# Optimization experiments

Measured on AMD Instinct MI355X. Metric: run time of the kernel, lower is better.

## Reference

```python
import math
import jax, jax.numpy as jnp
import numpy as np

D_MODEL = 1024
NUM_HEADS = 16
HEAD_DIM = D_MODEL // NUM_HEADS
MAX_REL = 128


def setup_inputs() -> dict:
    key = jax.random.key(0)
    ks = jax.random.split(key, 7)
    B, S = 2, 2048
    s = 1.0 / math.sqrt(D_MODEL)
    return {
        "x": jax.random.normal(ks[0], (B, S, D_MODEL), dtype=jnp.float32),
        "mask": jnp.ones((B, S, S), dtype=jnp.int32),
        "w_q": jax.random.normal(ks[1], (D_MODEL, D_MODEL), dtype=jnp.float32) * s,
        "w_k": jax.random.normal(ks[2], (D_MODEL, D_MODEL), dtype=jnp.float32) * s,
        "w_v": jax.random.normal(ks[3], (D_MODEL, D_MODEL), dtype=jnp.float32) * s,
        "w_o_w": jax.random.normal(ks[4], (D_MODEL, D_MODEL), dtype=jnp.float32) * s,
        "w_o_b": jnp.zeros((D_MODEL,), dtype=jnp.float32),
        "rel_emb": jax.random.normal(ks[5], (2 * MAX_REL + 1, HEAD_DIM), dtype=jnp.float32),
    }


def reference(x, mask, w_q, w_k, w_v, w_o_w, w_o_b, rel_emb):
    B, S, D = x.shape
    H, hd = NUM_HEADS, HEAD_DIM
    scale = math.sqrt(hd)

    def proj(w):  # torch Linear: x @ w.T  -> [B,H,S,hd]
        return (x @ w.T).reshape(B, S, H, hd).transpose(0, 2, 1, 3)

    Q, K, V = proj(w_q), proj(w_k), proj(w_v)

    # content scores (scaled)
    scores = jnp.einsum("bhqd,bhkd->bhqk", Q, K) / scale

    # T5-style relative position bias (NOT scaled, matching source)
    pos = jnp.arange(S)
    dist = jnp.clip(pos[None, :] - pos[:, None], -MAX_REL, MAX_REL) + MAX_REL  # [S,S]
    rel = rel_emb[dist]  # [S,S,hd]
    scores = scores + jnp.einsum("bhqd,qkd->bhqk", Q, rel)

    scores = jnp.where(mask[:, None, :, :] == 0, -1e9, scores)
    attn = jax.nn.softmax(scores, axis=-1)  # [B,H,S,S]

    ctx = jnp.einsum("bhqk,bhkd->bhqd", attn, V)
    ctx = ctx.transpose(0, 2, 1, 3).reshape(B, S, D)
    out = ctx @ w_o_w.T + w_o_b
    return out, attn
```

## Files before the change

kernel.cpp:

```cpp
#include <hip/hip_runtime.h>
#include <hip/hip_bf16.h>

#define B_ 2
#define S_ 2048
#define H_ 16
#define HD_ 64
#define D_ 1024
#define NJ_ 257
#define RSTRIDE_ 264

typedef __bf16 v8bf __attribute__((ext_vector_type(8)));
typedef __bf16 v4bf __attribute__((ext_vector_type(4)));
typedef float  v4f  __attribute__((ext_vector_type(4)));

static __device__ __forceinline__ v4f mfma16(v8bf a, v8bf b, v4f c) {
    return __builtin_amdgcn_mfma_f32_16x16x32_bf16(a, b, c, 0, 0, 0);
}

__global__ void k_split2(const float* __restrict__ src, __bf16* __restrict__ h,
                         __bf16* __restrict__ l, int n4) {
    int i = blockIdx.x * blockDim.x + threadIdx.x;
    int stride = gridDim.x * blockDim.x;
    for (; i < n4; i += stride) {
        const float4 v = ((const float4*)src)[i];
        float vv[4] = {v.x, v.y, v.z, v.w};
        v4bf hv, lv;
#pragma unroll
        for (int j = 0; j < 4; j++) {
            __bf16 hb = (__bf16)vv[j];
            hv[j] = hb;
            lv[j] = (__bf16)(vv[j] - (float)hb);
        }
        *(v4bf*)(h + 4 * (size_t)i) = hv;
        *(v4bf*)(l + 4 * (size_t)i) = lv;
    }
}

__global__ void k_cast4(const float* __restrict__ w0, const float* __restrict__ w1,
                        const float* __restrict__ w2, const float* __restrict__ w3,
                        __bf16* __restrict__ o0, __bf16* __restrict__ o1,
                        __bf16* __restrict__ o2, __bf16* __restrict__ o3) {
    const int n4each = (D_ * D_) / 4;
    int i = blockIdx.x * blockDim.x + threadIdx.x;
    int stride = gridDim.x * blockDim.x;
    for (; i < 4 * n4each; i += stride) {
        const int region = i >> 18, j = i & (n4each - 1);
        const float* src = region == 0 ? w0 : region == 1 ? w1 : region == 2 ? w2 : w3;
        __bf16* dst = region == 0 ? o0 : region == 1 ? o1 : region == 2 ? o2 : o3;
        const float4 v = ((const float4*)src)[j];
        v4bf o = {(__bf16)v.x, (__bf16)v.y, (__bf16)v.z, (__bf16)v.w};
        *(v4bf*)(dst + 4 * (size_t)j) = o;
    }
}

__global__ void k_rowflag(const int* __restrict__ mask, unsigned char* __restrict__ flags) {
    const int row = blockIdx.x;
    const int4* mp = (const int4*)(mask + (size_t)row * S_);
    int ok = 1;
    for (int i = threadIdx.x; i < S_ / 4; i += blockDim.x) {
        int4 m = mp[i];
        ok &= (m.x != 0) & (m.y != 0) & (m.z != 0) & (m.w != 0);
    }
    int all = __syncthreads_and(ok);
    if (threadIdx.x == 0) flags[row] = (unsigned char)(all != 0);
}

__global__ __launch_bounds__(256) void k_projQKV(const __bf16* __restrict__ xh,
                                                 const __bf16* __restrict__ xl,
                                                 const __bf16* __restrict__ wqh,
                                                 const __bf16* __restrict__ wkh,
                                                 const __bf16* __restrict__ wvh,
                                                 __bf16* __restrict__ Qh,
                                                 __bf16* __restrict__ Ql,
                                                 __bf16* __restrict__ Kh,
                                                 __bf16* __restrict__ Vb) {
    __shared__ __bf16 sXh[64][72], sXl[64][72], sW[64][72];
    const int seg = blockIdx.x >> 4;
    const int n0 = (blockIdx.x & 15) * 64;
    const int m0 = blockIdx.y * 64;
    const __bf16* W = seg == 0 ? wqh : (seg == 1 ? wkh : wvh);
    const int tid = threadIdx.x, lane = tid & 63, wid = tid >> 6;
    const int fr = lane & 15, fo = (lane >> 4) * 8;
    const int srow = tid >> 2, scol = (tid & 3) * 16;
    v4f acc[4] = {};
    for (int k0 = 0; k0 < D_; k0 += 64) {
        const size_t ga = (size_t)(m0 + srow) * D_ + k0 + scol;
        const size_t gb = (size_t)(n0 + srow) * D_ + k0 + scol;
        *(v8bf*)&sXh[srow][scol]     = *(const v8bf*)(xh + ga);
        *(v8bf*)&sXh[srow][scol + 8] = *(const v8bf*)(xh + ga + 8);
        if (seg < 2) {
            *(v8bf*)&sXl[srow][scol]     = *(const v8bf*)(xl + ga);
            *(v8bf*)&sXl[srow][scol + 8] = *(const v8bf*)(xl + ga + 8);
        }
        *(v8bf*)&sW[srow][scol]     = *(const v8bf*)(W + gb);
        *(v8bf*)&sW[srow][scol + 8] = *(const v8bf*)(W + gb + 8);
        __syncthreads();
#pragma unroll
        for (int ks = 0; ks < 2; ks++) {
            v8bf ah = *(const v8bf*)&sXh[wid * 16 + fr][ks * 32 + fo];
            v8bf al;
            if (seg < 2) al = *(const v8bf*)&sXl[wid * 16 + fr][ks * 32 + fo];
#pragma unroll
            for (int nt = 0; nt < 4; nt++) {
                v8bf bb = *(const v8bf*)&sW[nt * 16 + fr][ks * 32 + fo];
                acc[nt] = mfma16(ah, bb, acc[nt]);
                if (seg < 2) acc[nt] = mfma16(al, bb, acc[nt]);
            }
        }
        __syncthreads();
    }
#pragma unroll
    for (int nt = 0; nt < 4; nt++) {
#pragma unroll
        for (int r = 0; r < 4; r++) {
            const int row = m0 + wid * 16 + (lane >> 4) * 4 + r;
            const int col = n0 + nt * 16 + fr;
            const size_t idx = (size_t)row * D_ + col;
            const float f = acc[nt][r];
            if (seg == 0) {
                __bf16 hb = (__bf16)f;
                Qh[idx] = hb;
                Ql[idx] = (__bf16)(f - (float)hb);
            } else if (seg == 1) {
                Kh[idx] = (__bf16)f;
            } else {
                Vb[idx] = (__bf16)f;
            }
        }
    }
}

__global__ __launch_bounds__(256) void k_vtrans(const __bf16* __restrict__ Vb,
                                                __bf16* __restrict__ Vt) {
    __shared__ __bf16 t[64][72];
    const int s0 = blockIdx.x * 64, n0 = blockIdx.y * 64, b = blockIdx.z;
    const int tid = threadIdx.x;
    const int r = tid >> 2, c = (tid & 3) * 16;
    const size_t gin = ((size_t)(b * S_ + s0 + r)) * D_ + n0 + c;
    *(v8bf*)&t[r][c]     = *(const v8bf*)(Vb + gin);
    *(v8bf*)&t[r][c + 8] = *(const v8bf*)(Vb + gin + 8);
    __syncthreads();
    v8bf o0, o1;
#pragma unroll
    for (int j = 0; j < 8; j++) { o0[j] = t[c + j][r]; o1[j] = t[c + 8 + j][r]; }
    const size_t gout = ((size_t)(b * D_ + n0 + r)) * S_ + s0 + c;
    *(v8bf*)(Vt + gout)     = o0;
    *(v8bf*)(Vt + gout + 8) = o1;
}

__global__ __launch_bounds__(256) void k_relgemm(const __bf16* __restrict__ Qh,
                                                 const __bf16* __restrict__ Ql,
                                                 const __bf16* __restrict__ relh,
                                                 const __bf16* __restrict__ rell,
                                                 float* __restrict__ Rg,
                                                 float* __restrict__ qnorm,
                                                 float* __restrict__ Rmax) {
    const int q0 = blockIdx.x * 64;
    const int bh = blockIdx.y;
    const int b = bh >> 4, h = bh & 15;
    const int tid = threadIdx.x, lane = tid & 63, wid = tid >> 6;
    const int fr = lane & 15, fo = (lane >> 4) * 8;
    const size_t qbase = (size_t)(b * S_ + q0 + wid * 16 + fr) * D_ + h * HD_;
    v8bf qa_h[2], qa_l[2];
#pragma unroll
    for (int ks = 0; ks < 2; ks++) {
        qa_h[ks] = *(const v8bf*)(Qh + qbase + ks * 32 + fo);
        qa_l[ks] = *(const v8bf*)(Ql + qbase + ks * 32 + fo);
    }

    float qs = 0.0f;
#pragma unroll
    for (int ks = 0; ks < 2; ks++)
#pragma unroll
        for (int j = 0; j < 8; j++) {
            const float v = (float)qa_h[ks][j] + (float)qa_l[ks][j];
            qs += v * v;
        }
    qs += __shfl_xor(qs, 16);
    qs += __shfl_xor(qs, 32);
    if ((lane >> 4) == 0) qnorm[(size_t)bh * S_ + q0 + wid * 16 + fr] = sqrtf(qs);

    v4f acc[17] = {};
#pragma unroll
    for (int jt = 0; jt < 17; jt++) {
        int j = jt * 16 + fr;
        if (j > 256) j = 256;
        const size_t rb = (size_t)j * HD_;
#pragma unroll
        for (int ks = 0; ks < 2; ks++) {
            v8bf bh_ = *(const v8bf*)(relh + rb + ks * 32 + fo);
            v8bf bl_ = *(const v8bf*)(rell + rb + ks * 32 + fo);
            acc[jt] = mfma16(qa_h[ks], bh_, acc[jt]);
            acc[jt] = mfma16(qa_h[ks], bl_, acc[jt]);
            acc[jt] = mfma16(qa_l[ks], bh_, acc[jt]);
        }
    }

    float rm[4] = {-3.0e38f, -3.0e38f, -3.0e38f, -3.0e38f};
#pragma unroll
    for (int jt = 0; jt < 17; jt++)
#pragma unroll
        for (int r = 0; r < 4; r++) rm[r] = fmaxf(rm[r], acc[jt][r]);
#pragma unroll
    for (int r = 0; r < 4; r++) {
#pragma unroll
        for (int sh = 1; sh < 16; sh <<= 1) rm[r] = fmaxf(rm[r], __shfl_xor(rm[r], sh));
    }
    if (fr == 0) {
#pragma unroll
        for (int r = 0; r < 4; r++)
            Rmax[(size_t)bh * S_ + q0 + wid * 16 + (lane >> 4) * 4 + r] = rm[r];
    }

    const size_t rowbase = ((size_t)bh * S_ + q0 + wid * 16 + (lane >> 4) * 4) * RSTRIDE_;
#pragma unroll
    for (int jt = 0; jt < 17; jt++) {
        const int j = jt * 16 + fr;
        if (j <= 256) {
#pragma unroll
            for (int r = 0; r < 4; r++)
                Rg[rowbase + (size_t)r * RSTRIDE_ + j] = acc[jt][r];
        }
    }
}

__global__ __launch_bounds__(256) void k_knorm(const __bf16* __restrict__ Kh,
                                               float* __restrict__ Kmax) {
    __shared__ float red[4];
    const int bh = blockIdx.x, b = bh >> 4, h = bh & 15;
    const int tid = threadIdx.x;
    float best = 0.0f;
#pragma unroll
    for (int i = 0; i < 8; i++) {
        const int k = tid + i * 256;
        const __bf16* kr = Kh + (size_t)(b * S_ + k) * D_ + h * HD_;
        float s = 0.0f;
#pragma unroll
        for (int j = 0; j < 8; j++) {
            v8bf v = *(const v8bf*)(kr + j * 8);
#pragma unroll
            for (int e = 0; e < 8; e++) { const float f = (float)v[e]; s += f * f; }
        }
        best = fmaxf(best, s);
    }
#pragma unroll
    for (int sh = 1; sh < 64; sh <<= 1) best = fmaxf(best, __shfl_xor(best, sh));
    if ((tid & 63) == 0) red[tid >> 6] = best;
    __syncthreads();
    if (tid == 0)
        Kmax[bh] = sqrtf(fmaxf(fmaxf(red[0], red[1]), fmaxf(red[2], red[3])));
}

__global__ __launch_bounds__(512, 4) void k_attnE(const __bf16* __restrict__ Qh,
                                                  const __bf16* __restrict__ Ql,
                                                  const __bf16* __restrict__ Kh,
                                                  const __bf16* __restrict__ Vt,
                                                  const float* __restrict__ Rg,
                                                  const int* __restrict__ mask,
                                                  const unsigned char* __restrict__ flags,
                                                  const float* __restrict__ qnorm,
                                                  const float* __restrict__ Rmax,
                                                  const float* __restrict__ Kmax,
                                                  __bf16* __restrict__ E,
                                                  float* __restrict__ attn,
                                                  __bf16* __restrict__ ctx) {
    __shared__ __bf16 sK[2][64][72], sV[2][64][72], sP[128][72];
    __shared__ float sLi[128];
    const int flat = blockIdx.x;
    const int swz = (flat & 7) * 64 + (flat >> 3);
    const int qt = swz & 15, bh = swz >> 4;
    const int b = bh >> 4, h = bh & 15;
    const int q0 = qt * 128;
    const int tid = threadIdx.x, lane = tid & 63, w = tid >> 6;
    const int fr = lane & 15, fq = lane >> 4, fo = fq * 8;
    const int myrow = w * 16 + fq * 4;
    const int srow = tid >> 3, sc8 = (tid & 7) * 8;

    const size_t qbase = (size_t)(b * S_ + q0 + w * 16 + fr) * D_ + h * HD_;
    v8bf qa_h[2], qa_l[2];
#pragma unroll
    for (int ks = 0; ks < 2; ks++) {
        qa_h[ks] = *(const v8bf*)(Qh + qbase + ks * 32 + fo);
        qa_l[ks] = *(const v8bf*)(Ql + qbase + ks * 32 + fo);
    }

    const int qg0 = q0 + myrow;
    const size_t rbase0 = ((size_t)bh * S_ + qg0) * RSTRIDE_;
    const size_t mbase0 = ((size_t)b * S_ + qg0) * S_;
    float rcL[4], rcR[4], mhat[4];
    int flr[4];
    const float km = Kmax[bh] * 0.125f;
#pragma unroll
    for (int r = 0; r < 4; r++) {
        rcL[r] = Rg[rbase0 + (size_t)r * RSTRIDE_];
        rcR[r] = Rg[rbase0 + (size_t)r * RSTRIDE_ + 256];
        flr[r] = flags[(size_t)b * S_ + qg0 + r];
        mhat[r] = Rmax[(size_t)bh * S_ + qg0 + r] +
                  qnorm[(size_t)bh * S_ + qg0 + r] * km + 0.5f;
    }

    const int erow = w * 16 + (lane >> 2);
    const int ecol = (lane & 3) * 16;
    __bf16* ebase = E + ((size_t)bh * S_ + q0 + erow) * S_ + ecol;

    const __bf16* kgbase = Kh + (size_t)(b * S_ + srow) * D_ + h * HD_ + sc8;
    const __bf16* vgbase = Vt + (size_t)(b * D_ + h * HD_ + srow) * S_ + sc8;
    v8bf rk = *(const v8bf*)(kgbase);
    v8bf rv = *(const v8bf*)(vgbase);
    *(v8bf*)&sK[0][srow][sc8] = rk;
    *(v8bf*)&sV[0][srow][sc8] = rv;
    rk = *(const v8bf*)(kgbase + (size_t)64 * D_);
    rv = *(const v8bf*)(vgbase + 64);
    __syncthreads();

    float lrun[4] = {0.0f, 0.0f, 0.0f, 0.0f};
    v4f acc2[4] = {};
    int cur = 0;
    for (int kc = 0; kc < 32; kc++) {
        const int k0 = kc * 64;
        v4f acc[4] = {};
#pragma unroll
        for (int ct = 0; ct < 4; ct++) {
#pragma unroll
            for (int ks = 0; ks < 2; ks++) {
                v8bf kb = *(const v8bf*)&sK[cur][ct * 16 + fr][ks * 32 + fo];
                acc[ct] = mfma16(qa_h[ks], kb, acc[ct]);
                acc[ct] = mfma16(qa_l[ks], kb, acc[ct]);
            }
        }
        const bool band = (kc >= 2 * qt - 3) && (kc <= 2 * qt + 3);
        const bool left = kc < 2 * qt;
#pragma unroll
        for (int r = 0; r < 4; r++) {
            const int qg = qg0 + r;
#pragma unroll
            for (int ct = 0; ct < 4; ct++) {
                const int k = k0 + ct * 16 + fr;
                float bias;
                if (band) {
                    const int dd = k - qg;
                    const int j = dd < -128 ? 0 : (dd > 128 ? 256 : dd + 128);
                    bias = Rg[rbase0 + (size_t)r * RSTRIDE_ + j];
                } else {
                    bias = left ? rcL[r] : rcR[r];
                }
                float sv = acc[ct][r] * 0.125f + bias;
                if (!flr[r] && mask[mbase0 + (size_t)r * S_ + k] == 0) sv = -1e9f;
                const float e = __expf(sv - mhat[r]);
                lrun[r] += e;
                sP[myrow + r][ct * 16 + fr] = (__bf16)e;
            }
        }
#pragma unroll
        for (int ks = 0; ks < 2; ks++) {
            v8bf pa = *(const v8bf*)&sP[w * 16 + fr][ks * 32 + fo];
#pragma unroll
            for (int ct = 0; ct < 4; ct++) {
                v8bf vb = *(const v8bf*)&sV[cur][ct * 16 + fr][ks * 32 + fo];
                acc2[ct] = mfma16(pa, vb, acc2[ct]);
            }
        }
        *(v8bf*)(ebase + k0)     = *(const v8bf*)&sP[erow][ecol];
        *(v8bf*)(ebase + k0 + 8) = *(const v8bf*)&sP[erow][ecol + 8];
        if (kc < 31) {
            *(v8bf*)&sK[cur ^ 1][srow][sc8] = rk;
            *(v8bf*)&sV[cur ^ 1][srow][sc8] = rv;
        }
        if (kc < 30) {
            rk = *(const v8bf*)(kgbase + (size_t)(k0 + 128) * D_);
            rv = *(const v8bf*)(vgbase + k0 + 128);
        }
        __syncthreads();
        cur ^= 1;
    }

    float invl[4];
#pragma unroll
    for (int r = 0; r < 4; r++) {
#pragma unroll
        for (int sh = 1; sh < 16; sh <<= 1) lrun[r] += __shfl_xor(lrun[r], sh);
        invl[r] = 1.0f / (lrun[r] + 1e-37f);
    }
    if (fr == 0) {
#pragma unroll
        for (int r = 0; r < 4; r++) sLi[myrow + r] = invl[r];
    }

#pragma unroll
    for (int ct = 0; ct < 4; ct++) {
#pragma unroll
        for (int r = 0; r < 4; r++) {
            const int qg = qg0 + r;
            const int d = ct * 16 + fr;
            ctx[(size_t)(b * S_ + qg) * D_ + h * HD_ + d] = (__bf16)(acc2[ct][r] * invl[r]);
        }
    }

    __syncthreads();

    const __bf16* Eblk = E + ((size_t)bh * S_ + q0) * S_;
    float* ablk = attn + ((size_t)bh * S_ + q0) * S_;
#pragma unroll 4
    for (int it = 0; it < 64; it++) {
        const int g = tid + it * 512;
        const int row = g >> 8;
        const int col8 = (g & 255) * 8;
        const float inv = sLi[row];
        const v8bf e = *(const v8bf*)(Eblk + (size_t)row * S_ + col8);
        float4 o0, o1;
        o0.x = (float)e[0] * inv; o0.y = (float)e[1] * inv;
        o0.z = (float)e[2] * inv; o0.w = (float)e[3] * inv;
        o1.x = (float)e[4] * inv; o1.y = (float)e[5] * inv;
        o1.z = (float)e[6] * inv; o1.w = (float)e[7] * inv;
        *(float4*)(ablk + (size_t)row * S_ + col8)     = o0;
        *(float4*)(ablk + (size_t)row * S_ + col8 + 4) = o1;
    }
}

__global__ __launch_bounds__(256) void k_outproj(const __bf16* __restrict__ A,
                                                 const __bf16* __restrict__ Bw,
                                                 const float* __restrict__ bias,
                                                 float* __restrict__ out) {
    __shared__ __bf16 sA[64][72], sB[64][72];
    const int n0 = blockIdx.x * 64;
    const int m0 = blockIdx.y * 64;
    const int tid = threadIdx.x, lane = tid & 63, wid = tid >> 6;
    const int fr = lane & 15, fo = (lane >> 4) * 8;
    const int srow = tid >> 2, scol = (tid & 3) * 16;
    v4f acc[4] = {};
    for (int k0 = 0; k0 < D_; k0 += 64) {
        const size_t ga = (size_t)(m0 + srow) * D_ + k0 + scol;
        const size_t gb = (size_t)(n0 + srow) * D_ + k0 + scol;
        *(v8bf*)&sA[srow][scol]     = *(const v8bf*)(A + ga);
        *(v8bf*)&sA[srow][scol + 8] = *(const v8bf*)(A + ga + 8);
        *(v8bf*)&sB[srow][scol]     = *(const v8bf*)(Bw + gb);
        *(v8bf*)&sB[srow][scol + 8] = *(const v8bf*)(Bw + gb + 8);
        __syncthreads();
#pragma unroll
        for (int ks = 0; ks < 2; ks++) {
            v8bf a = *(const v8bf*)&sA[wid * 16 + fr][ks * 32 + fo];
#pragma unroll
            for (int nt = 0; nt < 4; nt++) {
                v8bf bb = *(const v8bf*)&sB[nt * 16 + fr][ks * 32 + fo];
                acc[nt] = mfma16(a, bb, acc[nt]);
            }
        }
        __syncthreads();
    }
#pragma unroll
    for (int nt = 0; nt < 4; nt++) {
        const float bv = bias[n0 + nt * 16 + fr];
#pragma unroll
        for (int r = 0; r < 4; r++) {
            const int row = m0 + wid * 16 + (lane >> 4) * 4 + r;
            out[(size_t)row * D_ + n0 + nt * 16 + fr] = acc[nt][r] + bv;
        }
    }
}

extern "C" void kernel_launch(void* const* d_in, const int* in_sizes, int n_in,
                              void* d_out, int out_size, void* d_ws, size_t ws_size,
                              hipStream_t stream) {
    (void)in_sizes; (void)n_in; (void)out_size; (void)ws_size;
    const float* x    = (const float*)d_in[0];
    const int*   mask = (const int*)d_in[1];
    const float* wq   = (const float*)d_in[2];
    const float* wk   = (const float*)d_in[3];
    const float* wv   = (const float*)d_in[4];
    const float* wo   = (const float*)d_in[5];
    const float* wob  = (const float*)d_in[6];
    const float* rel  = (const float*)d_in[7];
    float* out  = (float*)d_out;
    float* attn = out + (size_t)B_ * S_ * D_;

    char* p = (char*)d_ws;
    auto alloc = [&](size_t bytes) -> char* {
        char* r = p;
        p += (bytes + 255) & ~(size_t)255;
        return r;
    };
    const size_t BSD = (size_t)B_ * S_ * D_;
    const size_t DD  = (size_t)D_ * D_;
    const size_t BHS = (size_t)B_ * H_ * S_;
    __bf16* xh   = (__bf16*)alloc(BSD * 2);
    __bf16* xl   = (__bf16*)alloc(BSD * 2);
    __bf16* wqh  = (__bf16*)alloc(DD * 2);
    __bf16* wkh  = (__bf16*)alloc(DD * 2);
    __bf16* wvh  = (__bf16*)alloc(DD * 2);
    __bf16* woh  = (__bf16*)alloc(DD * 2);
    __bf16* relh = (__bf16*)alloc((size_t)NJ_ * HD_ * 2);
    __bf16* rell = (__bf16*)alloc((size_t)NJ_ * HD_ * 2);
    __bf16* Qh   = (__bf16*)alloc(BSD * 2);
    __bf16* Ql   = (__bf16*)alloc(BSD * 2);
    __bf16* Kh   = (__bf16*)alloc(BSD * 2);
    __bf16* Vb   = (__bf16*)alloc(BSD * 2);
    __bf16* Vt   = (__bf16*)alloc(BSD * 2);
    float*  Rg   = (float*)alloc(BHS * RSTRIDE_ * 4);
    float*  qn   = (float*)alloc(BHS * 4);
    float*  Rmax = (float*)alloc(BHS * 4);
    float*  Kmax = (float*)alloc((size_t)B_ * H_ * 4);
    __bf16* E    = (__bf16*)alloc((size_t)B_ * H_ * S_ * S_ * 2);
    __bf16* ctx  = (__bf16*)alloc(BSD * 2);
    unsigned char* flags = (unsigned char*)alloc((size_t)B_ * S_);

    k_split2<<<2048, 256, 0, stream>>>(x, xh, xl, (int)(BSD / 4));
    k_split2<<<17, 256, 0, stream>>>(rel, relh, rell, (int)(NJ_ * HD_ / 4));
    k_cast4<<<1024, 256, 0, stream>>>(wq, wk, wv, wo, wqh, wkh, wvh, woh);

    k_rowflag<<<B_ * S_, 256, 0, stream>>>(mask, flags);

    k_projQKV<<<dim3(48, B_ * S_ / 64), 256, 0, stream>>>(xh, xl, wqh, wkh, wvh,
                                                          Qh, Ql, Kh, Vb);

    k_vtrans<<<dim3(S_ / 64, D_ / 64, B_), 256, 0, stream>>>(Vb, Vt);

    k_relgemm<<<dim3(S_ / 64, B_ * H_), 256, 0, stream>>>(Qh, Ql, relh, rell, Rg, qn, Rmax);

    k_knorm<<<B_ * H_, 256, 0, stream>>>(Kh, Kmax);

    k_attnE<<<512, 512, 0, stream>>>(Qh, Ql, Kh, Vt, Rg, mask, flags, qn, Rmax, Kmax,
                                     E, attn, ctx);

    k_outproj<<<dim3(D_ / 64, B_ * S_ / 64), 256, 0, stream>>>(ctx, woh, wob, out);
}
```

Measured before the change: 560.1 us.

## Split attention key tiles across wave pairs with 64-row query tiles

The attention kernel now processes 64 query rows per block instead of 128. Each pair of waves splits the 64-key chunk between them, and partial PV accumulators and row sums are merged through shared memory at the end. The grid doubles to 1024 blocks, K/V staging goes from double to single buffering with an extra barrier per chunk, launch bounds ask for 8 blocks per CU, and shared-memory row padding changes from 72 to 76 across several kernels. This is meant to raise occupancy and parallelism, at the cost of more barriers, merge overhead and losing the overlap between loading K/V and computing.

Result: slower. 1.028 ms (+83.6%).

```diff
diff --git a/kernel.cpp b/kernel.cpp
--- a/kernel.cpp
+++ b/kernel.cpp
@@ -74,7 +74,7 @@
                                                  __bf16* __restrict__ Ql,
                                                  __bf16* __restrict__ Kh,
                                                  __bf16* __restrict__ Vb) {
-    __shared__ __bf16 sXh[64][72], sXl[64][72], sW[64][72];
+    __shared__ __bf16 sXh[64][76], sXl[64][76], sW[64][76];
     const int seg = blockIdx.x >> 4;
     const int n0 = (blockIdx.x & 15) * 64;
     const int m0 = blockIdx.y * 64;
@@ -132,7 +132,7 @@
 
 __global__ __launch_bounds__(256) void k_vtrans(const __bf16* __restrict__ Vb,
                                                 __bf16* __restrict__ Vt) {
-    __shared__ __bf16 t[64][72];
+    __shared__ __bf16 t[64][76];
     const int s0 = blockIdx.x * 64, n0 = blockIdx.y * 64, b = blockIdx.z;
     const int tid = threadIdx.x;
     const int r = tid >> 2, c = (tid & 3) * 16;
@@ -251,7 +251,7 @@
         Kmax[bh] = sqrtf(fmaxf(fmaxf(red[0], red[1]), fmaxf(red[2], red[3])));
 }
 
-__global__ __launch_bounds__(512, 4) void k_attnE(const __bf16* __restrict__ Qh,
+__global__ __launch_bounds__(512, 8) void k_attnE(const __bf16* __restrict__ Qh,
                                                   const __bf16* __restrict__ Ql,
                                                   const __bf16* __restrict__ Kh,
                                                   const __bf16* __restrict__ Vt,
@@ -264,19 +264,22 @@
                                                   __bf16* __restrict__ E,
                                                   float* __restrict__ attn,
                                                   __bf16* __restrict__ ctx) {
-    __shared__ __bf16 sK[2][64][72], sV[2][64][72], sP[128][72];
-    __shared__ float sLi[128];
+    __shared__ __bf16 sK[64][76], sV[64][76], sP[64][76];
+    __shared__ float sMrg[32][66];
+    __shared__ float sLsum[2][64];
+    __shared__ float sLi[64];
     const int flat = blockIdx.x;
-    const int swz = (flat & 7) * 64 + (flat >> 3);
-    const int qt = swz & 15, bh = swz >> 4;
+    const int swz = (flat & 7) * 128 + (flat >> 3);
+    const int qt = swz & 31, bh = swz >> 5;
     const int b = bh >> 4, h = bh & 15;
-    const int q0 = qt * 128;
+    const int q0 = qt * 64;
     const int tid = threadIdx.x, lane = tid & 63, w = tid >> 6;
+    const int wr = w >> 1, wc = w & 1;
     const int fr = lane & 15, fq = lane >> 4, fo = fq * 8;
-    const int myrow = w * 16 + fq * 4;
+    const int myrow = wr * 16 + fq * 4;
     const int srow = tid >> 3, sc8 = (tid & 7) * 8;
 
-    const size_t qbase = (size_t)(b * S_ + q0 + w * 16 + fr) * D_ + h * HD_;
+    const size_t qbase = (size_t)(b * S_ + q0 + wr * 16 + fr) * D_ + h * HD_;
     v8bf qa_h[2], qa_l[2];
 #pragma unroll
     for (int ks = 0; ks < 2; ks++) {
@@ -299,43 +302,42 @@
                   qnorm[(size_t)bh * S_ + qg0 + r] * km + 0.5f;
     }
 
-    const int erow = w * 16 + (lane >> 2);
-    const int ecol = (lane & 3) * 16;
-    __bf16* ebase = E + ((size_t)bh * S_ + q0 + erow) * S_ + ecol;
+    const int erow = wr * 16 + (lane >> 2);
+    const int ec = wc * 32 + (lane & 3) * 8;
+    __bf16* ebase = E + ((size_t)bh * S_ + q0 + erow) * S_ + ec;
 
     const __bf16* kgbase = Kh + (size_t)(b * S_ + srow) * D_ + h * HD_ + sc8;
     const __bf16* vgbase = Vt + (size_t)(b * D_ + h * HD_ + srow) * S_ + sc8;
     v8bf rk = *(const v8bf*)(kgbase);
     v8bf rv = *(const v8bf*)(vgbase);
-    *(v8bf*)&sK[0][srow][sc8] = rk;
-    *(v8bf*)&sV[0][srow][sc8] = rv;
+    *(v8bf*)&sK[srow][sc8] = rk;
+    *(v8bf*)&sV[srow][sc8] = rv;
     rk = *(const v8bf*)(kgbase + (size_t)64 * D_);
     rv = *(const v8bf*)(vgbase + 64);
     __syncthreads();
 
     float lrun[4] = {0.0f, 0.0f, 0.0f, 0.0f};
     v4f acc2[4] = {};
-    int cur = 0;
     for (int kc = 0; kc < 32; kc++) {
         const int k0 = kc * 64;
-        v4f acc[4] = {};
-#pragma unroll
-        for (int ct = 0; ct < 4; ct++) {
+        v4f acc[2] = {};
+#pragma unroll
+        for (int ct = 0; ct < 2; ct++) {
 #pragma unroll
             for (int ks = 0; ks < 2; ks++) {
-                v8bf kb = *(const v8bf*)&sK[cur][ct * 16 + fr][ks * 32 + fo];
+                v8bf kb = *(const v8bf*)&sK[wc * 32 + ct * 16 + fr][ks * 32 + fo];
                 acc[ct] = mfma16(qa_h[ks], kb, acc[ct]);
                 acc[ct] = mfma16(qa_l[ks], kb, acc[ct]);
             }
         }
-        const bool band = (kc >= 2 * qt - 3) && (kc <= 2 * qt + 3);
-        const bool left = kc < 2 * qt;
+        const bool band = (kc >= qt - 2) && (kc <= qt + 2);
+        const bool left = kc < qt;
 #pragma unroll
         for (int r = 0; r < 4; r++) {
             const int qg = qg0 + r;
 #pragma unroll
-            for (int ct = 0; ct < 4; ct++) {
-                const int k = k0 + ct * 16 + fr;
+            for (int ct = 0; ct < 2; ct++) {
+                const int k = k0 + wc * 32 + ct * 16 + fr;
                 float bias;
                 if (band) {
                     const int dd = k - qg;
@@ -348,60 +350,78 @@
                 if (!flr[r] && mask[mbase0 + (size_t)r * S_ + k] == 0) sv = -1e9f;
                 const float e = __expf(sv - mhat[r]);
                 lrun[r] += e;
-                sP[myrow + r][ct * 16 + fr] = (__bf16)e;
-            }
-        }
-#pragma unroll
-        for (int ks = 0; ks < 2; ks++) {
-            v8bf pa = *(const v8bf*)&sP[w * 16 + fr][ks * 32 + fo];
-#pragma unroll
-            for (int ct = 0; ct < 4; ct++) {
-                v8bf vb = *(const v8bf*)&sV[cur][ct * 16 + fr][ks * 32 + fo];
-                acc2[ct] = mfma16(pa, vb, acc2[ct]);
-            }
-        }
-        *(v8bf*)(ebase + k0)     = *(const v8bf*)&sP[erow][ecol];
-        *(v8bf*)(ebase + k0 + 8) = *(const v8bf*)&sP[erow][ecol + 8];
+                sP[myrow + r][wc * 32 + ct * 16 + fr] = (__bf16)e;
+            }
+        }
+        *(v8bf*)(ebase + k0) = *(const v8bf*)&sP[erow][ec];
+        {
+            v8bf pa = *(const v8bf*)&sP[wr * 16 + fr][wc * 32 + fo];
+#pragma unroll
+            for (int ct2 = 0; ct2 < 4; ct2++) {
+                v8bf vb = *(const v8bf*)&sV[ct2 * 16 + fr][wc * 32 + fo];
+                acc2[ct2] = mfma16(pa, vb, acc2[ct2]);
+            }
+        }
         if (kc < 31) {
-            *(v8bf*)&sK[cur ^ 1][srow][sc8] = rk;
-            *(v8bf*)&sV[cur ^ 1][srow][sc8] = rv;
-        }
-        if (kc < 30) {
-            rk = *(const v8bf*)(kgbase + (size_t)(k0 + 128) * D_);
-            rv = *(const v8bf*)(vgbase + k0 + 128);
+            __syncthreads();
+            *(v8bf*)&sK[srow][sc8] = rk;
+            *(v8bf*)&sV[srow][sc8] = rv;
+            if (kc < 30) {
+                rk = *(const v8bf*)(kgbase + (size_t)(k0 + 128) * D_);
+                rv = *(const v8bf*)(vgbase + k0 + 128);
+            }
+            __syncthreads();
+        }
+    }
+
+#pragma unroll
+    for (int r = 0; r < 4; r++) {
+#pragma unroll
+        for (int sh = 1; sh < 16; sh <<= 1) lrun[r] += __shfl_xor(lrun[r], sh);
+    }
+    if (fr == 0) {
+#pragma unroll
+        for (int r = 0; r < 4; r++) sLsum[wc][myrow + r] = lrun[r];
+    }
+    __syncthreads();
+    float invl[4];
+#pragma unroll
+    for (int r = 0; r < 4; r++)
+        invl[r] = 1.0f / (sLsum[0][myrow + r] + sLsum[1][myrow + r] + 1e-37f);
+    if (wc == 0 && fr == 0) {
+#pragma unroll
+        for (int r = 0; r < 4; r++) sLi[myrow + r] = invl[r];
+    }
+
+#pragma unroll
+    for (int m = 0; m < 2; m++) {
+        if (wc == 1 && (wr >> 1) == m) {
+#pragma unroll
+            for (int ct2 = 0; ct2 < 4; ct2++)
+#pragma unroll
+                for (int r = 0; r < 4; r++)
+                    sMrg[(wr & 1) * 16 + fq * 4 + r][ct2 * 16 + fr] = acc2[ct2][r];
         }
         __syncthreads();
-        cur ^= 1;
-    }
-
-    float invl[4];
-#pragma unroll
-    for (int r = 0; r < 4; r++) {
-#pragma unroll
-        for (int sh = 1; sh < 16; sh <<= 1) lrun[r] += __shfl_xor(lrun[r], sh);
-        invl[r] = 1.0f / (lrun[r] + 1e-37f);
-    }
-    if (fr == 0) {
-#pragma unroll
-        for (int r = 0; r < 4; r++) sLi[myrow + r] = invl[r];
-    }
-
-#pragma unroll
-    for (int ct = 0; ct < 4; ct++) {
-#pragma unroll
-        for (int r = 0; r < 4; r++) {
-            const int qg = qg0 + r;
-            const int d = ct * 16 + fr;
-            ctx[(size_t)(b * S_ + qg) * D_ + h * HD_ + d] = (__bf16)(acc2[ct][r] * invl[r]);
-        }
-    }
-
-    __syncthreads();
+        if (wc == 0 && (wr >> 1) == m) {
+#pragma unroll
+            for (int ct2 = 0; ct2 < 4; ct2++)
+#pragma unroll
+                for (int r = 0; r < 4; r++) {
+                    const float tot =
+                        acc2[ct2][r] + sMrg[(wr & 1) * 16 + fq * 4 + r][ct2 * 16 + fr];
+                    const int qg = qg0 + r;
+                    ctx[(size_t)(b * S_ + qg) * D_ + h * HD_ + ct2 * 16 + fr] =
+                        (__bf16)(tot * invl[r]);
+                }
+        }
+        __syncthreads();
+    }
 
     const __bf16* Eblk = E + ((size_t)bh * S_ + q0) * S_;
     float* ablk = attn + ((size_t)bh * S_ + q0) * S_;
 #pragma unroll 4
-    for (int it = 0; it < 64; it++) {
+    for (int it = 0; it < 32; it++) {
         const int g = tid + it * 512;
         const int row = g >> 8;
         const int col8 = (g & 255) * 8;
@@ -421,7 +441,7 @@
                                                  const __bf16* __restrict__ Bw,
                                                  const float* __restrict__ bias,
                                                  float* __restrict__ out) {
-    __shared__ __bf16 sA[64][72], sB[64][72];
+    __shared__ __bf16 sA[64][76], sB[64][76];
     const int n0 = blockIdx.x * 64;
     const int m0 = blockIdx.y * 64;
     const int tid = threadIdx.x, lane = tid & 63, wid = tid >> 6;
@@ -518,8 +538,8 @@
 
     k_knorm<<<B_ * H_, 256, 0, stream>>>(Kh, Kmax);
 
-    k_attnE<<<512, 512, 0, stream>>>(Qh, Ql, Kh, Vt, Rg, mask, flags, qn, Rmax, Kmax,
-                                     E, attn, ctx);
+    k_attnE<<<1024, 512, 0, stream>>>(Qh, Ql, Kh, Vt, Rg, mask, flags, qn, Rmax, Kmax,
+                                      E, attn, ctx);
 
     k_outproj<<<dim3(D_ / 64, B_ * S_ / 64), 256, 0, stream>>>(ctx, woh, wob, out);
 }
```
